# Kernel tuning notes

Measured on AMD Instinct MI355X. Metric: run time of the kernel, lower is better.

Reference implementation:

```python
import jax, jax.numpy as jnp
import numpy as np

N = 4096
F_IN = 8
H = 64


def setup_inputs() -> dict:
    key = jax.random.key(0)
    ks = jax.random.split(key, 12)
    s_in = 1.0 / np.sqrt(F_IN)
    s_h = 1.0 / np.sqrt(2 * H)
    inp = {
        "node_features": jax.random.normal(ks[0], (N, F_IN), dtype=jnp.float32),
        "adjacency_matrix": jax.random.uniform(ks[1], (N, N), dtype=jnp.float32),
        # nn.Linear weights are (out, in)
        "W_enc": jax.random.uniform(ks[2], (H, F_IN), jnp.float32, -s_in, s_in),
        "b_enc": jax.random.uniform(ks[3], (H,), jnp.float32, -s_in, s_in),
        "W1": jax.random.uniform(ks[4], (H, 2 * H), jnp.float32, -s_h, s_h),
        "b1": jax.random.uniform(ks[5], (H,), jnp.float32, -s_h, s_h),
        "W2": jax.random.uniform(ks[6], (H, 2 * H), jnp.float32, -s_h, s_h),
        "b2": jax.random.uniform(ks[7], (H,), jnp.float32, -s_h, s_h),
        "W3": jax.random.uniform(ks[8], (H, 2 * H), jnp.float32, -s_h, s_h),
        "b3": jax.random.uniform(ks[9], (H,), jnp.float32, -s_h, s_h),
        "W_edge": jax.random.uniform(ks[10], (1, 2 * H), jnp.float32, -s_h, s_h),
        "b_edge": jax.random.uniform(ks[11], (1,), jnp.float32, -s_h, s_h),
    }
    return inp


def reference(node_features, adjacency_matrix, W_enc, b_enc, W1, b1, W2, b2, W3, b3, W_edge, b_edge):
    h = jax.nn.relu(node_features @ W_enc.T + b_enc)  # [N, H]
    for W, b in ((W1, b1), (W2, b2), (W3, b3)):
        h_neighbors = adjacency_matrix @ h            # [N, H]
        h_concat = jnp.concatenate([h, h_neighbors], axis=-1)  # [N, 2H]
        h = jax.nn.relu(h_concat @ W.T + b)
    # edge_scorer is linear: score[i,j] = w_i . h[i] + w_j . h[j] + b  (rank-1 decomposition,
    # avoids materializing the [N,N,2H] pairwise concat of the original double loop)
    w_i = W_edge[0, :H]   # [H]
    w_j = W_edge[0, H:]   # [H]
    s_i = h @ w_i         # [N]
    s_j = h @ w_j         # [N]
    scores = s_i[:, None] + s_j[None, :] + b_edge[0]  # [N, N]
    n = node_features.shape[0]
    scores = scores * (1.0 - jnp.eye(n, dtype=scores.dtype))  # diagonal stays 0
    return scores
```

## Files before the change

kernel.cpp:

```cpp
#include <hip/hip_runtime.h>

#define GN 4096
#define KS 8

typedef __attribute__((ext_vector_type(8))) short bf16x8_t;
typedef __attribute__((ext_vector_type(4))) float f32x4_t;

__device__ __forceinline__ short f2bf(float x) {
    union { float f; unsigned u; } c; c.f = x;
    unsigned r = (c.u + 0x7fffu + ((c.u >> 16) & 1u)) >> 16;
    return (short)r;
}

__global__ __launch_bounds__(256) void encoder_k(
    const float* __restrict__ X, const float* __restrict__ Wenc,
    const float* __restrict__ benc, float* __restrict__ h,
    short* __restrict__ Ht)
{
    const int g = blockIdx.x * 256 + threadIdx.x;
    const int i = g >> 6, f = g & 63;
    const float4 x0 = *(const float4*)(X + i * 8);
    const float4 x1 = *(const float4*)(X + i * 8 + 4);
    const float4 w0 = *(const float4*)(Wenc + f * 8);
    const float4 w1 = *(const float4*)(Wenc + f * 8 + 4);
    float acc = benc[f]
              + x0.x * w0.x + x0.y * w0.y + x0.z * w0.z + x0.w * w0.w
              + x1.x * w1.x + x1.y * w1.y + x1.z * w1.z + x1.w * w1.w;
    acc = fmaxf(acc, 0.f);
    h[g] = acc;
    Ht[f * GN + i] = f2bf(acc);
}

__global__ __launch_bounds__(256) void gemm_ah(
    const float* __restrict__ A, const short* __restrict__ Ht,
    float* __restrict__ part, int ks_len)
{
    __shared__ short Al[4 * 64 * 8];
    __shared__ short Bl[4 * 64 * 8];

    const int t  = threadIdx.x;
    const int ks = blockIdx.x;
    const int mt = blockIdx.y << 6;
    const int kb = ks * ks_len;

    const int row_ld = t >> 2;
    const int p_ld   = t & 3;

    const float* aP = A  + (size_t)(mt + row_ld) * GN + kb + p_ld * 8;
    const short* bP = Ht + row_ld * GN + kb + p_ld * 8;
    short* AlW = &Al[(p_ld * 64 + row_ld) * 8];
    short* BlW = &Bl[(p_ld * 64 + row_ld) * 8];

    const int w = t >> 6, lane = t & 63;
    const int quad = lane >> 4, l16 = lane & 15;
    const short* AlR = &Al[(quad * 64 + w * 16 + l16) * 8];
    const short* BlR = &Bl[(quad * 64 + l16) * 8];

    f32x4_t acc0 = {0.f, 0.f, 0.f, 0.f};
    f32x4_t acc1 = acc0, acc2 = acc0, acc3 = acc0;

    float4 a0 = *(const float4*)aP;
    float4 a1 = *(const float4*)(aP + 4);
    bf16x8_t bv = *(const bf16x8_t*)bP;

    for (int kk = 0; kk < ks_len; kk += 32) {
        bf16x8_t av;
        av[0] = f2bf(a0.x); av[1] = f2bf(a0.y);
        av[2] = f2bf(a0.z); av[3] = f2bf(a0.w);
        av[4] = f2bf(a1.x); av[5] = f2bf(a1.y);
        av[6] = f2bf(a1.z); av[7] = f2bf(a1.w);
        *(bf16x8_t*)AlW = av;
        *(bf16x8_t*)BlW = bv;
        __syncthreads();
        if (kk + 32 < ks_len) {
            aP += 32; bP += 32;
            a0 = *(const float4*)aP;
            a1 = *(const float4*)(aP + 4);
            bv = *(const bf16x8_t*)bP;
        }
        bf16x8_t af = *(const bf16x8_t*)AlR;
        bf16x8_t b0 = *(const bf16x8_t*)(BlR);
        bf16x8_t b1 = *(const bf16x8_t*)(BlR + 16 * 8);
        bf16x8_t b2 = *(const bf16x8_t*)(BlR + 32 * 8);
        bf16x8_t b3 = *(const bf16x8_t*)(BlR + 48 * 8);
        acc0 = __builtin_amdgcn_mfma_f32_16x16x32_bf16(af, b0, acc0, 0, 0, 0);
        acc1 = __builtin_amdgcn_mfma_f32_16x16x32_bf16(af, b1, acc1, 0, 0, 0);
        acc2 = __builtin_amdgcn_mfma_f32_16x16x32_bf16(af, b2, acc2, 0, 0, 0);
        acc3 = __builtin_amdgcn_mfma_f32_16x16x32_bf16(af, b3, acc3, 0, 0, 0);
        __syncthreads();
    }

    float* o = part + ((size_t)ks * GN + mt + w * 16 + quad * 4) * 64 + l16;
    #pragma unroll
    for (int r = 0; r < 4; ++r) {
        o[r * 64 +  0] = acc0[r];
        o[r * 64 + 16] = acc1[r];
        o[r * 64 + 32] = acc2[r];
        o[r * 64 + 48] = acc3[r];
    }
}

__global__ __launch_bounds__(256) void dense_mlp(
    const float* __restrict__ hin, const float* __restrict__ part,
    const float* __restrict__ W, const float* __restrict__ bias,
    float* __restrict__ hout, short* __restrict__ HtOut,
    const float* __restrict__ Wedge,
    float* __restrict__ s_i, float* __restrict__ s_j, int last)
{
    __shared__ float hl[256];
    __shared__ float hnl[256];
    __shared__ float Wl[64 * 129];
    const int t = threadIdx.x;
    const int node0 = blockIdx.x * 4;

    {
        const int iloc = t >> 6, k = t & 63;
        const size_t idx = (size_t)(node0 + iloc) * 64 + k;
        hl[t] = hin[idx];
        float s = 0.f;
        #pragma unroll
        for (int p = 0; p < KS; ++p) s += part[(size_t)p * GN * 64 + idx];
        hnl[t] = s;
    }
    {
        #pragma unroll
        for (int o = 0; o < 8; ++o) {
            const int g = t * 4 + o * 1024;
            const float4 v = *(const float4*)(W + g);
            const int r = g >> 7, c = g & 127;
            float* d = &Wl[r * 129 + c];
            d[0] = v.x; d[1] = v.y; d[2] = v.z; d[3] = v.w;
        }
    }
    __syncthreads();

    const int iloc = t >> 6, f = t & 63;
    const int node = node0 + iloc;
    float acc = bias[f];
    const float* wrow  = &Wl[f * 129];
    const float* hrow  = &hl[iloc * 64];
    const float* hnrow = &hnl[iloc * 64];
    #pragma unroll
    for (int k = 0; k < 64; ++k) acc += hrow[k] * wrow[k];
    #pragma unroll
    for (int k = 0; k < 64; ++k) acc += hnrow[k] * wrow[64 + k];
    acc = fmaxf(acc, 0.f);

    if (!last) {
        hout[(size_t)node * 64 + f] = acc;
        HtOut[f * GN + node] = f2bf(acc);
    } else {
        float vi = acc * Wedge[f];
        float vj = acc * Wedge[64 + f];
        #pragma unroll
        for (int off = 32; off > 0; off >>= 1) {
            vi += __shfl_xor(vi, off, 64);
            vj += __shfl_xor(vj, off, 64);
        }
        if (f == 0) { s_i[node] = vi; s_j[node] = vj; }
    }
}

__global__ __launch_bounds__(256) void scores_k(
    const float* __restrict__ s_i, const float* __restrict__ s_j,
    const float* __restrict__ be, float* __restrict__ out)
{
    const int i  = blockIdx.y;
    const int j0 = (blockIdx.x * 256 + threadIdx.x) * 4;
    const float si = s_i[i] + be[0];
    const float4 sj = *(const float4*)(s_j + j0);
    float4 o = make_float4(si + sj.x, si + sj.y, si + sj.z, si + sj.w);
    const int d = i - j0;
    if (d >= 0 && d < 4) (&o.x)[d] = 0.f;
    *(float4*)(out + (size_t)i * GN + j0) = o;
}

extern "C" void kernel_launch(void* const* d_in, const int* in_sizes, int n_in,
                              void* d_out, int out_size, void* d_ws, size_t ws_size,
                              hipStream_t stream) {
    const float* X     = (const float*)d_in[0];
    const float* A     = (const float*)d_in[1];
    const float* Wenc  = (const float*)d_in[2];
    const float* benc  = (const float*)d_in[3];
    const float* Wmat[3] = {(const float*)d_in[4], (const float*)d_in[6], (const float*)d_in[8]};
    const float* bvec[3] = {(const float*)d_in[5], (const float*)d_in[7], (const float*)d_in[9]};
    const float* Wedge = (const float*)d_in[10];
    const float* bedge = (const float*)d_in[11];
    float* out = (float*)d_out;

    char* ws = (char*)d_ws;
    float* part = (float*)ws;
    float* h    = (float*)(ws + ((size_t)8 << 20));
    short* Ht   = (short*)(ws + ((size_t)9 << 20));
    float* s_i  = (float*)(ws + ((size_t)9 << 20) + (512u << 10));
    float* s_j  = s_i + GN;

    encoder_k<<<dim3(GN * 64 / 256), 256, 0, stream>>>(X, Wenc, benc, h, Ht);

    for (int r = 0; r < 3; ++r) {
        gemm_ah<<<dim3(KS, GN / 64), 256, 0, stream>>>(A, Ht, part, GN / KS);
        dense_mlp<<<dim3(GN / 4), 256, 0, stream>>>(
            h, part, Wmat[r], bvec[r], h, Ht, Wedge, s_i, s_j, r == 2);
    }

    scores_k<<<dim3(GN / 1024, GN), 256, 0, stream>>>(s_i, s_j, bedge, out);
}
```

Before: 221.8 us.

## Load GEMM operands directly to registers, use split-bf16 MFMA for dense MLP

The adjacency GEMM no longer stages tiles through LDS with barriers. Each wave loads its A rows and Ht columns straight from global memory into MFMA operand registers and packs the bf16 conversion pairwise. The dense layer becomes an MFMA kernel using a hi/lo bf16 split (three products) to keep near-fp32 accuracy, replacing the scalar LDS dot products. The edge projection moves into a separate small kernel, which adds one launch. The gain from dropping barriers and LDS traffic comes at the cost of lost cross-wave reuse of B and more redundant global loads.

```diff
diff --git a/kernel.cpp b/kernel.cpp
--- a/kernel.cpp
+++ b/kernel.cpp
@@ -6,10 +6,42 @@
 typedef __attribute__((ext_vector_type(8))) short bf16x8_t;
 typedef __attribute__((ext_vector_type(4))) float f32x4_t;
 
+__device__ __forceinline__ unsigned rne(unsigned u) {
+    return u + 0x7fffu + ((u >> 16) & 1u);
+}
+__device__ __forceinline__ unsigned pkbf(float x, float y) {
+    union { float f; unsigned u; } a, b; a.f = x; b.f = y;
+    return (rne(a.u) >> 16) | (rne(b.u) & 0xffff0000u);
+}
+__device__ __forceinline__ bf16x8_t cvt8(float4 a0, float4 a1) {
+    union { unsigned u[4]; bf16x8_t v; } r;
+    r.u[0] = pkbf(a0.x, a0.y);
+    r.u[1] = pkbf(a0.z, a0.w);
+    r.u[2] = pkbf(a1.x, a1.y);
+    r.u[3] = pkbf(a1.z, a1.w);
+    return r.v;
+}
 __device__ __forceinline__ short f2bf(float x) {
     union { float f; unsigned u; } c; c.f = x;
-    unsigned r = (c.u + 0x7fffu + ((c.u >> 16) & 1u)) >> 16;
-    return (short)r;
+    return (short)(rne(c.u) >> 16);
+}
+__device__ __forceinline__ float bf2f(short s) {
+    union { unsigned u; float f; } c; c.u = ((unsigned)(unsigned short)s) << 16;
+    return c.f;
+}
+__device__ __forceinline__ void split8(float4 a0, float4 a1, bf16x8_t& hi, bf16x8_t& lo) {
+    float v[8] = {a0.x, a0.y, a0.z, a0.w, a1.x, a1.y, a1.z, a1.w};
+    union { short s[8]; bf16x8_t t; } H, L;
+    #pragma unroll
+    for (int i = 0; i < 8; ++i) {
+        short h = f2bf(v[i]);
+        H.s[i] = h;
+        L.s[i] = f2bf(v[i] - bf2f(h));
+    }
+    hi = H.t; lo = L.t;
+}
+__device__ __forceinline__ void split8p(const float* p, bf16x8_t& hi, bf16x8_t& lo) {
+    split8(*(const float4*)p, *(const float4*)(p + 4), hi, lo);
 }
 
 __global__ __launch_bounds__(256) void encoder_k(
@@ -35,62 +67,34 @@
     const float* __restrict__ A, const short* __restrict__ Ht,
     float* __restrict__ part, int ks_len)
 {
-    __shared__ short Al[4 * 64 * 8];
-    __shared__ short Bl[4 * 64 * 8];
-
-    const int t  = threadIdx.x;
-    const int ks = blockIdx.x;
-    const int mt = blockIdx.y << 6;
-    const int kb = ks * ks_len;
-
-    const int row_ld = t >> 2;
-    const int p_ld   = t & 3;
-
-    const float* aP = A  + (size_t)(mt + row_ld) * GN + kb + p_ld * 8;
-    const short* bP = Ht + row_ld * GN + kb + p_ld * 8;
-    short* AlW = &Al[(p_ld * 64 + row_ld) * 8];
-    short* BlW = &Bl[(p_ld * 64 + row_ld) * 8];
-
+    const int t = threadIdx.x;
     const int w = t >> 6, lane = t & 63;
     const int quad = lane >> 4, l16 = lane & 15;
-    const short* AlR = &Al[(quad * 64 + w * 16 + l16) * 8];
-    const short* BlR = &Bl[(quad * 64 + l16) * 8];
+    const int m0 = (blockIdx.y << 6) + (w << 4);
+    const int kb = blockIdx.x * ks_len;
+
+    const float* aP = A  + (size_t)(m0 + l16) * GN + kb + quad * 8;
+    const short* bP = Ht + (size_t)l16 * GN + kb + quad * 8;
 
     f32x4_t acc0 = {0.f, 0.f, 0.f, 0.f};
     f32x4_t acc1 = acc0, acc2 = acc0, acc3 = acc0;
 
-    float4 a0 = *(const float4*)aP;
-    float4 a1 = *(const float4*)(aP + 4);
-    bf16x8_t bv = *(const bf16x8_t*)bP;
-
+    #pragma unroll 4
     for (int kk = 0; kk < ks_len; kk += 32) {
-        bf16x8_t av;
-        av[0] = f2bf(a0.x); av[1] = f2bf(a0.y);
-        av[2] = f2bf(a0.z); av[3] = f2bf(a0.w);
-        av[4] = f2bf(a1.x); av[5] = f2bf(a1.y);
-        av[6] = f2bf(a1.z); av[7] = f2bf(a1.w);
-        *(bf16x8_t*)AlW = av;
-        *(bf16x8_t*)BlW = bv;
-        __syncthreads();
-        if (kk + 32 < ks_len) {
-            aP += 32; bP += 32;
-            a0 = *(const float4*)aP;
-            a1 = *(const float4*)(aP + 4);
-            bv = *(const bf16x8_t*)bP;
-        }
-        bf16x8_t af = *(const bf16x8_t*)AlR;
-        bf16x8_t b0 = *(const bf16x8_t*)(BlR);
-        bf16x8_t b1 = *(const bf16x8_t*)(BlR + 16 * 8);
-        bf16x8_t b2 = *(const bf16x8_t*)(BlR + 32 * 8);
-        bf16x8_t b3 = *(const bf16x8_t*)(BlR + 48 * 8);
+        float4   a0 = *(const float4*)(aP + kk);
+        float4   a1 = *(const float4*)(aP + kk + 4);
+        bf16x8_t b0 = *(const bf16x8_t*)(bP + kk);
+        bf16x8_t b1 = *(const bf16x8_t*)(bP + kk + 16 * GN);
+        bf16x8_t b2 = *(const bf16x8_t*)(bP + kk + 32 * GN);
+        bf16x8_t b3 = *(const bf16x8_t*)(bP + kk + 48 * GN);
+        bf16x8_t af = cvt8(a0, a1);
         acc0 = __builtin_amdgcn_mfma_f32_16x16x32_bf16(af, b0, acc0, 0, 0, 0);
         acc1 = __builtin_amdgcn_mfma_f32_16x16x32_bf16(af, b1, acc1, 0, 0, 0);
         acc2 = __builtin_amdgcn_mfma_f32_16x16x32_bf16(af, b2, acc2, 0, 0, 0);
         acc3 = __builtin_amdgcn_mfma_f32_16x16x32_bf16(af, b3, acc3, 0, 0, 0);
-        __syncthreads();
-    }
-
-    float* o = part + ((size_t)ks * GN + mt + w * 16 + quad * 4) * 64 + l16;
+    }
+
+    float* o = part + ((size_t)blockIdx.x * GN + m0 + quad * 4) * 64 + l16;
     #pragma unroll
     for (int r = 0; r < 4; ++r) {
         o[r * 64 +  0] = acc0[r];
@@ -100,65 +104,95 @@
     }
 }
 
-__global__ __launch_bounds__(256) void dense_mlp(
+__global__ __launch_bounds__(64) void dense_split(
     const float* __restrict__ hin, const float* __restrict__ part,
     const float* __restrict__ W, const float* __restrict__ bias,
-    float* __restrict__ hout, short* __restrict__ HtOut,
-    const float* __restrict__ Wedge,
-    float* __restrict__ s_i, float* __restrict__ s_j, int last)
-{
-    __shared__ float hl[256];
-    __shared__ float hnl[256];
-    __shared__ float Wl[64 * 129];
+    float* __restrict__ hout, short* __restrict__ HtOut)
+{
+    const int lane = threadIdx.x & 63;
+    const int quad = lane >> 4, l16 = lane & 15;
+    const int m0 = blockIdx.x << 4;
+
+    f32x4_t acc0 = {0.f, 0.f, 0.f, 0.f};
+    f32x4_t acc1 = acc0, acc2 = acc0, acc3 = acc0;
+
+    #pragma unroll
+    for (int half = 0; half < 2; ++half) {
+        #pragma unroll
+        for (int kk = 0; kk < 64; kk += 32) {
+            const int kq = kk + quad * 8;
+            bf16x8_t ah, al;
+            if (half == 0) {
+                split8p(hin + (size_t)(m0 + l16) * 64 + kq, ah, al);
+            } else {
+                const size_t base = (size_t)(m0 + l16) * 64 + kq;
+                float4 s0 = make_float4(0.f, 0.f, 0.f, 0.f);
+                float4 s1 = make_float4(0.f, 0.f, 0.f, 0.f);
+                #pragma unroll
+                for (int p = 0; p < KS; ++p) {
+                    const float* pp = part + (size_t)p * (GN * 64) + base;
+                    float4 v0 = *(const float4*)pp;
+                    float4 v1 = *(const float4*)(pp + 4);
+                    s0.x += v0.x; s0.y += v0.y; s0.z += v0.z; s0.w += v0.w;
+                    s1.x += v1.x; s1.y += v1.y; s1.z += v1.z; s1.w += v1.w;
+                }
+                split8(s0, s1, ah, al);
+            }
+            const float* wp = W + half * 64 + kq;
+            bf16x8_t bh0, bl0, bh1, bl1, bh2, bl2, bh3, bl3;
+            split8p(wp + (size_t)(l16     ) * 128, bh0, bl0);
+            split8p(wp + (size_t)(l16 + 16) * 128, bh1, bl1);
+            split8p(wp + (size_t)(l16 + 32) * 128, bh2, bl2);
+            split8p(wp + (size_t)(l16 + 48) * 128, bh3, bl3);
+            acc0 = __builtin_amdgcn_mfma_f32_16x16x32_bf16(ah, bh0, acc0, 0, 0, 0);
+            acc0 = __builtin_amdgcn_mfma_f32_16x16x32_bf16(ah, bl0, acc0, 0, 0, 0);
+            acc0 = __builtin_amdgcn_mfma_f32_16x16x32_bf16(al, bh0, acc0, 0, 0, 0);
+            acc1 = __builtin_amdgcn_mfma_f32_16x16x32_bf16(ah, bh1, acc1, 0, 0, 0);
+            acc1 = __builtin_amdgcn_mfma_f32_16x16x32_bf16(ah, bl1, acc1, 0, 0, 0);
+            acc1 = __builtin_amdgcn_mfma_f32_16x16x32_bf16(al, bh1, acc1, 0, 0, 0);
+            acc2 = __builtin_amdgcn_mfma_f32_16x16x32_bf16(ah, bh2, acc2, 0, 0, 0);
+            acc2 = __builtin_amdgcn_mfma_f32_16x16x32_bf16(ah, bl2, acc2, 0, 0, 0);
+            acc2 = __builtin_amdgcn_mfma_f32_16x16x32_bf16(al, bh2, acc2, 0, 0, 0);
+            acc3 = __builtin_amdgcn_mfma_f32_16x16x32_bf16(ah, bh3, acc3, 0, 0, 0);
+            acc3 = __builtin_amdgcn_mfma_f32_16x16x32_bf16(ah, bl3, acc3, 0, 0, 0);
+            acc3 = __builtin_amdgcn_mfma_f32_16x16x32_bf16(al, bh3, acc3, 0, 0, 0);
+        }
+    }
+
+    const float bia0 = bias[l16], bia1 = bias[l16 + 16];
+    const float bia2 = bias[l16 + 32], bia3 = bias[l16 + 48];
+    #pragma unroll
+    for (int r = 0; r < 4; ++r) {
+        const int node = m0 + quad * 4 + r;
+        float v0 = fmaxf(acc0[r] + bia0, 0.f);
+        float v1 = fmaxf(acc1[r] + bia1, 0.f);
+        float v2 = fmaxf(acc2[r] + bia2, 0.f);
+        float v3 = fmaxf(acc3[r] + bia3, 0.f);
+        float* hp = hout + (size_t)node * 64 + l16;
+        hp[ 0] = v0; hp[16] = v1; hp[32] = v2; hp[48] = v3;
+        HtOut[(size_t)(l16     ) * GN + node] = f2bf(v0);
+        HtOut[(size_t)(l16 + 16) * GN + node] = f2bf(v1);
+        HtOut[(size_t)(l16 + 32) * GN + node] = f2bf(v2);
+        HtOut[(size_t)(l16 + 48) * GN + node] = f2bf(v3);
+    }
+}
+
+__global__ __launch_bounds__(256) void edge_k(
+    const float* __restrict__ h, const float* __restrict__ Wedge,
+    float* __restrict__ s_i, float* __restrict__ s_j)
+{
     const int t = threadIdx.x;
-    const int node0 = blockIdx.x * 4;
-
-    {
-        const int iloc = t >> 6, k = t & 63;
-        const size_t idx = (size_t)(node0 + iloc) * 64 + k;
-        hl[t] = hin[idx];
-        float s = 0.f;
-        #pragma unroll
-        for (int p = 0; p < KS; ++p) s += part[(size_t)p * GN * 64 + idx];
-        hnl[t] = s;
-    }
-    {
-        #pragma unroll
-        for (int o = 0; o < 8; ++o) {
-            const int g = t * 4 + o * 1024;
-            const float4 v = *(const float4*)(W + g);
-            const int r = g >> 7, c = g & 127;
-            float* d = &Wl[r * 129 + c];
-            d[0] = v.x; d[1] = v.y; d[2] = v.z; d[3] = v.w;
-        }
-    }
-    __syncthreads();
-
-    const int iloc = t >> 6, f = t & 63;
-    const int node = node0 + iloc;
-    float acc = bias[f];
-    const float* wrow  = &Wl[f * 129];
-    const float* hrow  = &hl[iloc * 64];
-    const float* hnrow = &hnl[iloc * 64];
-    #pragma unroll
-    for (int k = 0; k < 64; ++k) acc += hrow[k] * wrow[k];
-    #pragma unroll
-    for (int k = 0; k < 64; ++k) acc += hnrow[k] * wrow[64 + k];
-    acc = fmaxf(acc, 0.f);
-
-    if (!last) {
-        hout[(size_t)node * 64 + f] = acc;
-        HtOut[f * GN + node] = f2bf(acc);
-    } else {
-        float vi = acc * Wedge[f];
-        float vj = acc * Wedge[64 + f];
-        #pragma unroll
-        for (int off = 32; off > 0; off >>= 1) {
-            vi += __shfl_xor(vi, off, 64);
-            vj += __shfl_xor(vj, off, 64);
-        }
-        if (f == 0) { s_i[node] = vi; s_j[node] = vj; }
-    }
+    const int node = blockIdx.x * 4 + (t >> 6);
+    const int f = t & 63;
+    const float hv = h[(size_t)node * 64 + f];
+    float vi = hv * Wedge[f];
+    float vj = hv * Wedge[64 + f];
+    #pragma unroll
+    for (int off = 32; off > 0; off >>= 1) {
+        vi += __shfl_xor(vi, off, 64);
+        vj += __shfl_xor(vj, off, 64);
+    }
+    if (f == 0) { s_i[node] = vi; s_j[node] = vj; }
 }
 
 __global__ __launch_bounds__(256) void scores_k(
@@ -199,9 +233,10 @@
 
     for (int r = 0; r < 3; ++r) {
         gemm_ah<<<dim3(KS, GN / 64), 256, 0, stream>>>(A, Ht, part, GN / KS);
-        dense_mlp<<<dim3(GN / 4), 256, 0, stream>>>(
-            h, part, Wmat[r], bvec[r], h, Ht, Wedge, s_i, s_j, r == 2);
-    }
-
+        dense_split<<<dim3(GN / 16), 64, 0, stream>>>(
+            h, part, Wmat[r], bvec[r], h, Ht);
+    }
+
+    edge_k<<<dim3(GN / 4), 256, 0, stream>>>(h, Wedge, s_i, s_j);
     scores_k<<<dim3(GN / 1024, GN), 256, 0, stream>>>(s_i, s_j, bedge, out);
 }
```

Result: slower. 233.5 us (+5.3%).
